# Kernel tuning notes

Hardware: AMD Instinct MI355X
Metric: run time of the kernel (lower is better)

Reference implementation:

```python
import jax, jax.numpy as jnp
import numpy as np

N = 100000      # nodes
E = 1600000     # edges (avg degree 16)
EP = 500000     # pos/neg scored edges
DIN, DH, DOUT = 128, 128, 64


def setup_inputs() -> dict:
    key = jax.random.key(0)
    ks = jax.random.split(key, 8)
    x = jax.random.normal(ks[0], (N, DIN), jnp.float32)
    edge_index = jax.random.randint(ks[1], (2, E), 0, N)
    pos_edge_index = jax.random.randint(ks[2], (2, EP), 0, N)
    neg_edge_index = jax.random.randint(ks[3], (2, EP), 0, N)
    s = lambda k, sh: jax.random.normal(k, sh, jnp.float32) * 0.05
    return dict(
        x=x, edge_index=edge_index,
        pos_edge_index=pos_edge_index, neg_edge_index=neg_edge_index,
        W_l0=s(ks[4], (DIN, DH)), b_l0=jnp.zeros((DH,), jnp.float32), W_r0=s(ks[5], (DIN, DH)),
        W_l1=s(ks[6], (DH, DOUT)), b_l1=jnp.zeros((DOUT,), jnp.float32), W_r1=s(ks[7], (DH, DOUT)),
    )


def sage_conv(h, src, dst, W_l, b_l, W_r):
    # PyG SAGEConv (mean aggr): out_i = W_l @ mean_{j in N(i)} h_j + b_l + W_r @ h_i
    msg = h[src]                                                   # [E, d] gather
    agg = jax.ops.segment_sum(msg, dst, num_segments=h.shape[0])   # [N, d]
    deg = jax.ops.segment_sum(jnp.ones((src.shape[0],), h.dtype), dst, num_segments=h.shape[0])
    mean = agg / jnp.maximum(deg, 1.0)[:, None]
    return mean @ W_l + b_l + h @ W_r


def reference(x, edge_index, pos_edge_index, neg_edge_index,
              W_l0, b_l0, W_r0, W_l1, b_l1, W_r1):
    src, dst = edge_index[0], edge_index[1]
    h = sage_conv(x, src, dst, W_l0, b_l0, W_r0)
    h = jax.nn.relu(h)          # dropout is identity in eval mode
    h = sage_conv(h, src, dst, W_l1, b_l1, W_r1)
    pos_scores = (h[pos_edge_index[0]] * h[pos_edge_index[1]]).sum(axis=1)
    neg_scores = (h[neg_edge_index[0]] * h[neg_edge_index[1]]).sum(axis=1)
    return (pos_scores, neg_scores)
```

## Files before the change

### kernel.cpp

```cpp
#include <hip/hip_runtime.h>

#define NN 100000
#define EE 1600000
#define EPE 500000
#define NBINS 196
#define BCAP 12288
#define EPB 2048
#define NB1 782

typedef short bf8_t __attribute__((ext_vector_type(8)));
typedef float f4_t  __attribute__((ext_vector_type(4)));
typedef float f2v  __attribute__((ext_vector_type(2)));

__device__ __forceinline__ unsigned short f2bf(float f) {
    unsigned u = __float_as_uint(f);
    unsigned r = (u + 0x7fffu + ((u >> 16) & 1u)) >> 16;
    return (unsigned short)r;
}
__device__ __forceinline__ float bfl(unsigned u) { return __uint_as_float(u << 16); }
__device__ __forceinline__ float bfh(unsigned u) { return __uint_as_float(u & 0xffff0000u); }

__device__ __forceinline__ int c0p(int m) {
    return ((m >> 6) & 1) * 64 + (m & 3) * 16 + ((m >> 2) & 15);
}
__device__ __forceinline__ int c1p(int m) {
    return ((m >> 5) & 1) * 32 + (m & 1) * 16 + ((m >> 1) & 15);
}

#if __has_builtin(__builtin_amdgcn_cvt_pk_fp8_f32) && __has_builtin(__builtin_amdgcn_cvt_pk_f32_fp8)
__device__ __forceinline__ unsigned pk4_fp8(float a0, float a1, float a2, float a3) {
    int w = 0;
    w = __builtin_amdgcn_cvt_pk_fp8_f32(a0, a1, w, false);
    w = __builtin_amdgcn_cvt_pk_fp8_f32(a2, a3, w, true);
    return (unsigned)w;
}
__device__ __forceinline__ unsigned short pk2_fp8(float a0, float a1) {
    int w = __builtin_amdgcn_cvt_pk_fp8_f32(a0, a1, 0, false);
    return (unsigned short)(w & 0xffff);
}
__device__ __forceinline__ void accf8(float* a, uint2 v) {
    f2v p0 = __builtin_amdgcn_cvt_pk_f32_fp8((int)v.x, false);
    f2v p1 = __builtin_amdgcn_cvt_pk_f32_fp8((int)v.x, true);
    f2v p2 = __builtin_amdgcn_cvt_pk_f32_fp8((int)v.y, false);
    f2v p3 = __builtin_amdgcn_cvt_pk_f32_fp8((int)v.y, true);
    a[0] += p0.x; a[1] += p0.y; a[2] += p1.x; a[3] += p1.y;
    a[4] += p2.x; a[5] += p2.y; a[6] += p3.x; a[7] += p3.y;
}
#else
#include <hip/hip_fp8.h>
__device__ __forceinline__ unsigned pk4_fp8(float a0, float a1, float a2, float a3) {
    unsigned r;
    r  = (unsigned)__hip_cvt_float_to_fp8(a0, __HIP_SATFINITE, __HIP_E4M3);
    r |= (unsigned)__hip_cvt_float_to_fp8(a1, __HIP_SATFINITE, __HIP_E4M3) << 8;
    r |= (unsigned)__hip_cvt_float_to_fp8(a2, __HIP_SATFINITE, __HIP_E4M3) << 16;
    r |= (unsigned)__hip_cvt_float_to_fp8(a3, __HIP_SATFINITE, __HIP_E4M3) << 24;
    return r;
}
__device__ __forceinline__ unsigned short pk2_fp8(float a0, float a1) {
    unsigned r;
    r  = (unsigned)__hip_cvt_float_to_fp8(a0, __HIP_SATFINITE, __HIP_E4M3);
    r |= (unsigned)__hip_cvt_float_to_fp8(a1, __HIP_SATFINITE, __HIP_E4M3) << 8;
    return (unsigned short)r;
}
__device__ __forceinline__ float dec1_fp8(unsigned b) {
    __hip_fp8_e4m3 h; h.__x = (__hip_fp8_storage_t)(b & 0xff);
    return (float)h;
}
__device__ __forceinline__ void accf8(float* a, uint2 v) {
    a[0] += dec1_fp8(v.x); a[1] += dec1_fp8(v.x >> 8);
    a[2] += dec1_fp8(v.x >> 16); a[3] += dec1_fp8(v.x >> 24);
    a[4] += dec1_fp8(v.y); a[5] += dec1_fp8(v.y >> 8);
    a[6] += dec1_fp8(v.y >> 16); a[7] += dec1_fp8(v.y >> 24);
}
#endif

__global__ __launch_bounds__(256) void binpass1_k(
    const int* __restrict__ src, const int* __restrict__ dst,
    int* __restrict__ bin_cnt, int* __restrict__ binbuf)
{
    __shared__ int cnt_l[NBINS];
    __shared__ int base_l[NBINS];
    int tid = threadIdx.x;
    int e0 = blockIdx.x * EPB;
    for (int i = tid; i < NBINS; i += 256) cnt_l[i] = 0;
    __syncthreads();

    int pk[8];
    #pragma unroll
    for (int i = 0; i < 8; ++i) {
        int e = e0 + tid + i * 256;
        pk[i] = -1;
        if (e < EE) {
            int d = dst[e];
            int b = d >> 9;
            int r = atomicAdd(&cnt_l[b], 1);
            pk[i] = (b << 20) | ((d & 511) << 11) | r;
        }
    }
    __syncthreads();
    for (int i = tid; i < NBINS; i += 256)
        base_l[i] = atomicAdd(&bin_cnt[i], cnt_l[i]);
    __syncthreads();

    #pragma unroll
    for (int i = 0; i < 8; ++i) {
        int e = e0 + tid + i * 256;
        if (e >= EE) continue;
        int v = pk[i];
        int b = v >> 20, dl = (v >> 11) & 511, r = v & 2047;
        binbuf[b * BCAP + base_l[b] + r] = (dl << 17) | src[e];
    }
}

__global__ __launch_bounds__(256) void binpass2_k(
    const int* __restrict__ binbuf, const int* __restrict__ bin_cnt,
    int* __restrict__ csr, int* __restrict__ row_ptr, float* __restrict__ invd)
{
    __shared__ int deg_l[512];
    __shared__ int off_l[512];
    __shared__ int cur_l[512];
    __shared__ int s[256];
    int tid = threadIdx.x;
    int b = blockIdx.x;
    int lo = b << 9;
    int n_here = min(512, NN - lo);

    int bc = (tid < NBINS) ? bin_cnt[tid] : 0;
    s[tid] = bc;
    __syncthreads();
    #pragma unroll
    for (int off = 1; off < 256; off <<= 1) {
        int t = (tid >= off) ? s[tid - off] : 0;
        __syncthreads();
        s[tid] += t;
        __syncthreads();
    }
    int base = (b == 0) ? 0 : s[b - 1];
    int cnt = bin_cnt[b];
    const int* bb = binbuf + b * BCAP;
    __syncthreads();

    deg_l[tid] = 0; deg_l[tid + 256] = 0;
    __syncthreads();
    for (int i = tid; i < cnt; i += 256)
        atomicAdd(&deg_l[bb[i] >> 17], 1);
    __syncthreads();

    int a0 = deg_l[2 * tid], a1 = deg_l[2 * tid + 1];
    s[tid] = a0 + a1;
    __syncthreads();
    #pragma unroll
    for (int off = 1; off < 256; off <<= 1) {
        int t = (tid >= off) ? s[tid - off] : 0;
        __syncthreads();
        s[tid] += t;
        __syncthreads();
    }
    int excl = s[tid] - (a0 + a1);
    off_l[2 * tid] = excl;
    off_l[2 * tid + 1] = excl + a0;
    cur_l[2 * tid] = excl;
    cur_l[2 * tid + 1] = excl + a0;
    __syncthreads();

    for (int j = tid; j < n_here; j += 256) {
        row_ptr[lo + j] = base + off_l[j];
        invd[lo + j] = 1.0f / fmaxf((float)deg_l[j], 1.0f);
    }
    if (tid == 0 && b == NBINS - 1) row_ptr[NN] = EE;

    for (int i = tid; i < cnt; i += 256) {
        int v = bb[i];
        int dstl = v >> 17, srcv = v & 0x1FFFF;
        int pos = atomicAdd(&cur_l[dstl], 1);
        csr[base + pos] = srcv;
    }
}

__global__ void pack_k(const float* __restrict__ Wl0, const float* __restrict__ Wr0,
                       const float* __restrict__ Wl1, const float* __restrict__ Wr1,
                       const float* __restrict__ bl0, const float* __restrict__ bl1,
                       unsigned short* __restrict__ Bp0, unsigned short* __restrict__ Bp1,
                       float* __restrict__ b0p, float* __restrict__ b1p,
                       int* __restrict__ bin_cnt)
{
    int t = blockIdx.x * 256 + threadIdx.x;
    if (t < NBINS) bin_cnt[t] = 0;
    if (t < 4096) {
        int q = t & 3;
        int n = (t >> 2) & 255;
        int kt = t >> 10;
        unsigned short o[8];
        #pragma unroll
        for (int j = 0; j < 8; ++j) {
            int k = kt * 32 + q * 8 + j;
            float v = (n < 128) ? Wl0[(size_t)k * 128 + n] : Wr0[(size_t)k * 128 + (n - 128)];
            o[j] = f2bf(v);
        }
        uint4 w;
        w.x = (unsigned)o[0] | ((unsigned)o[1] << 16);
        w.y = (unsigned)o[2] | ((unsigned)o[3] << 16);
        w.z = (unsigned)o[4] | ((unsigned)o[5] << 16);
        w.w = (unsigned)o[6] | ((unsigned)o[7] << 16);
        *(uint4*)(Bp0 + (size_t)t * 8) = w;
    } else if (t < 6144) {
        int u = t - 4096;
        int q = u & 3;
        int n = (u >> 2) & 127;
        int kt = u >> 9;
        unsigned short o[8];
        #pragma unroll
        for (int j = 0; j < 8; ++j) {
            int k = kt * 32 + q * 8 + j;
            int c = c0p(k);
            float v = (n < 64) ? Wl1[(size_t)c * 64 + n] : Wr1[(size_t)c * 64 + (n - 64)];
            o[j] = f2bf(v);
        }
        uint4 w;
        w.x = (unsigned)o[0] | ((unsigned)o[1] << 16);
        w.y = (unsigned)o[2] | ((unsigned)o[3] << 16);
        w.z = (unsigned)o[4] | ((unsigned)o[5] << 16);
        w.w = (unsigned)o[6] | ((unsigned)o[7] << 16);
        *(uint4*)(Bp1 + (size_t)u * 8) = w;
    } else if (t < 6144 + 128) {
        int m = t - 6144;
        b0p[m] = bl0[c0p(m)];
    } else if (t < 6144 + 192) {
        int m = t - 6272;
        b1p[m] = bl1[c1p(m)];
    }
}

template<int NCOLS, bool AFP32>
__global__ __launch_bounds__(256) void gemm_k(
    const void* __restrict__ Av, const unsigned short* __restrict__ Bp,
    unsigned char* __restrict__ Tout, unsigned short* __restrict__ Rout)
{
    constexpr int STRIP = NCOLS / 4;
    constexpr int NT = STRIP / 16;
    constexpr int HC = NCOLS / 2;
    int w = threadIdx.x >> 6;
    int lane = threadIdx.x & 63;
    int ln = lane & 15, q = lane >> 4;
    int half = w >> 1, wsub = w & 1;
    int row0 = blockIdx.x * 64;
    int colbase = half * HC + wsub * STRIP;

    bf8_t Bf[4][NT];
    #pragma unroll
    for (int kt = 0; kt < 4; ++kt)
        #pragma unroll
        for (int nt = 0; nt < NT; ++nt)
            Bf[kt][nt] = *(const bf8_t*)(Bp + (size_t)kt * NCOLS * 32
                                         + (size_t)(colbase + nt * 16 + ln) * 32 + q * 8);

    for (int rt = 0; rt < 4; ++rt) {
        int rowt = row0 + rt * 16;
        if (rowt >= NN) break;
        int arow = rowt + ln;

        bf8_t Af[4];
        if (AFP32) {
            #pragma unroll
            for (int kt = 0; kt < 4; ++kt) {
                const float* ap = (const float*)Av + (size_t)arow * 128 + kt * 32 + q * 8;
                f4_t a0 = *(const f4_t*)ap;
                f4_t a1 = *(const f4_t*)(ap + 4);
                #pragma unroll
                for (int j = 0; j < 4; ++j) {
                    Af[kt][j]     = (short)f2bf(a0[j]);
                    Af[kt][4 + j] = (short)f2bf(a1[j]);
                }
            }
        } else {
            #pragma unroll
            for (int kt = 0; kt < 4; ++kt)
                Af[kt] = *(const bf8_t*)((const unsigned short*)Av
                                         + (size_t)arow * 128 + kt * 32 + q * 8);
        }

        f4_t acc[NT];
        #pragma unroll
        for (int nt = 0; nt < NT; ++nt) acc[nt] = (f4_t){0.f, 0.f, 0.f, 0.f};
        #pragma unroll
        for (int kt = 0; kt < 4; ++kt)
            #pragma unroll
            for (int nt = 0; nt < NT; ++nt)
                acc[nt] = __builtin_amdgcn_mfma_f32_16x16x32_bf16(Af[kt], Bf[kt][nt], acc[nt], 0, 0, 0);

        #pragma unroll
        for (int r = 0; r < 4; ++r) {
            int row = rowt + q * 4 + r;
            if (half == 0) {
                if (NT == 4) {
                    unsigned v = pk4_fp8(acc[0][r], acc[1][r], acc[2][r], acc[3][r]);
                    *(unsigned*)(Tout + (size_t)row * HC + wsub * 64 + ln * 4) = v;
                } else {
                    unsigned short v = pk2_fp8(acc[0][r], acc[1][r]);
                    *(unsigned short*)(Tout + (size_t)row * HC + wsub * 32 + ln * 2) = v;
                }
            } else {
                if (NT == 4) {
                    uint2 v;
                    v.x = (unsigned)f2bf(acc[0][r]) | ((unsigned)f2bf(acc[1][r]) << 16);
                    v.y = (unsigned)f2bf(acc[2][r]) | ((unsigned)f2bf(acc[3][r]) << 16);
                    *(uint2*)(Rout + (size_t)row * HC + wsub * 64 + ln * 4) = v;
                } else {
                    unsigned v = (unsigned)f2bf(acc[0][r]) | ((unsigned)f2bf(acc[1][r]) << 16);
                    *(unsigned*)(Rout + (size_t)row * HC + wsub * 32 + ln * 2) = v;
                }
            }
        }
    }
}

__device__ __forceinline__ void unp8(float* a, uint4 v) {
    a[0] = bfl(v.x); a[1] = bfh(v.x);
    a[2] = bfl(v.y); a[3] = bfh(v.y);
    a[4] = bfl(v.z); a[5] = bfh(v.z);
    a[6] = bfl(v.w); a[7] = bfh(v.w);
}

template<int LPNS, bool RELU>
__global__ __launch_bounds__(256) void gather_fuse_k(
    const unsigned char* __restrict__ tq, const int* __restrict__ csr,
    const int* __restrict__ row_ptr, const float* __restrict__ invd,
    const unsigned short* __restrict__ rg, const float* __restrict__ biasp,
    unsigned short* __restrict__ hout)
{
    constexpr int STRIDE = 8 << LPNS;
    int t = blockIdx.x * 256 + threadIdx.x;
    int node = t >> LPNS;
    int lane = t & ((1 << LPNS) - 1);
    if (node >= NN) return;
    int e = row_ptr[node];
    int e1 = row_ptr[node + 1];
    const unsigned char* fb = tq + lane * 8;

    float a0[8] = {0.f, 0.f, 0.f, 0.f, 0.f, 0.f, 0.f, 0.f};
    float a1[8] = {0.f, 0.f, 0.f, 0.f, 0.f, 0.f, 0.f, 0.f};
    for (; e + 3 < e1; e += 4) {
        int s0 = csr[e], s1 = csr[e + 1], s2 = csr[e + 2], s3 = csr[e + 3];
        uint2 v0 = *(const uint2*)(fb + (size_t)s0 * STRIDE);
        uint2 v1 = *(const uint2*)(fb + (size_t)s1 * STRIDE);
        uint2 v2 = *(const uint2*)(fb + (size_t)s2 * STRIDE);
        uint2 v3 = *(const uint2*)(fb + (size_t)s3 * STRIDE);
        accf8(a0, v0); accf8(a1, v1); accf8(a0, v2); accf8(a1, v3);
    }
    for (; e < e1; ++e) {
        int s0 = csr[e];
        uint2 v0 = *(const uint2*)(fb + (size_t)s0 * STRIDE);
        accf8(a0, v0);
    }

    float inv = invd[node];
    uint4 rv = *(const uint4*)(rg + (size_t)node * STRIDE + lane * 8);
    float rr[8];
    unp8(rr, rv);
    f4_t b0 = *(const f4_t*)(biasp + lane * 8);
    f4_t b1 = *(const f4_t*)(biasp + lane * 8 + 4);
    float o[8];
    #pragma unroll
    for (int j = 0; j < 8; ++j) {
        float bj = (j < 4) ? b0[j] : b1[j - 4];
        float v = (a0[j] + a1[j]) * inv + rr[j] + bj;
        o[j] = RELU ? fmaxf(v, 0.f) : v;
    }
    uint4 w;
    w.x = (unsigned)f2bf(o[0]) | ((unsigned)f2bf(o[1]) << 16);
    w.y = (unsigned)f2bf(o[2]) | ((unsigned)f2bf(o[3]) << 16);
    w.z = (unsigned)f2bf(o[4]) | ((unsigned)f2bf(o[5]) << 16);
    w.w = (unsigned)f2bf(o[6]) | ((unsigned)f2bf(o[7]) << 16);
    *(uint4*)(hout + (size_t)node * STRIDE + lane * 8) = w;
}

__device__ __forceinline__ float dot8(uint4 va, uint4 vb) {
    return bfl(va.x) * bfl(vb.x) + bfh(va.x) * bfh(vb.x)
         + bfl(va.y) * bfl(vb.y) + bfh(va.y) * bfh(vb.y)
         + bfl(va.z) * bfl(vb.z) + bfh(va.z) * bfh(vb.z)
         + bfl(va.w) * bfl(vb.w) + bfh(va.w) * bfh(vb.w);
}

__global__ __launch_bounds__(256) void score_k(
    const unsigned short* __restrict__ h2b, const int* __restrict__ pos,
    const int* __restrict__ neg, float* __restrict__ out)
{
    int t = blockIdx.x * 256 + threadIdx.x;
    int g = t >> 3, l = t & 7;
    int eg0 = g * 2;
    if (eg0 >= 2 * EPE) return;
    int eg1 = eg0 + 1;
    int a0i, b0i, a1i, b1i;
    if (eg0 < EPE) { a0i = pos[eg0]; b0i = pos[EPE + eg0]; }
    else { int e2 = eg0 - EPE; a0i = neg[e2]; b0i = neg[EPE + e2]; }
    if (eg1 < EPE) { a1i = pos[eg1]; b1i = pos[EPE + eg1]; }
    else { int e2 = eg1 - EPE; a1i = neg[e2]; b1i = neg[EPE + e2]; }
    const unsigned short* hb = h2b + (size_t)l * 8;
    uint4 va0 = *(const uint4*)(hb + (size_t)a0i * 64);
    uint4 vb0 = *(const uint4*)(hb + (size_t)b0i * 64);
    uint4 va1 = *(const uint4*)(hb + (size_t)a1i * 64);
    uint4 vb1 = *(const uint4*)(hb + (size_t)b1i * 64);
    float p0 = dot8(va0, vb0);
    float p1 = dot8(va1, vb1);
    p0 += __shfl_xor(p0, 1, 8);
    p1 += __shfl_xor(p1, 1, 8);
    p0 += __shfl_xor(p0, 2, 8);
    p1 += __shfl_xor(p1, 2, 8);
    p0 += __shfl_xor(p0, 4, 8);
    p1 += __shfl_xor(p1, 4, 8);
    if (l == 0) { out[eg0] = p0; out[eg1] = p1; }
}

extern "C" void kernel_launch(void* const* d_in, const int* in_sizes, int n_in,
                              void* d_out, int out_size, void* d_ws, size_t ws_size,
                              hipStream_t stream) {
    const float* x   = (const float*)d_in[0];
    const int*   ei  = (const int*)d_in[1];
    const int*   pei = (const int*)d_in[2];
    const int*   nei = (const int*)d_in[3];
    const float* Wl0 = (const float*)d_in[4];
    const float* bl0 = (const float*)d_in[5];
    const float* Wr0 = (const float*)d_in[6];
    const float* Wl1 = (const float*)d_in[7];
    const float* bl1 = (const float*)d_in[8];
    const float* Wr1 = (const float*)d_in[9];
    float* out = (float*)d_out;

    char* ws = (char*)d_ws;
    size_t off = 0;
    auto alloc = [&](size_t bytes) {
        void* p = ws + off;
        off = (off + bytes + 255) & ~(size_t)255;
        return p;
    };
    float* invd     = (float*)alloc((size_t)NN * 4);
    int*   row_ptr  = (int*)  alloc((size_t)(NN + 1) * 4);
    int*   bin_cnt  = (int*)  alloc((size_t)NBINS * 4);
    int*   binbuf   = (int*)  alloc((size_t)NBINS * BCAP * 4);
    int*   csr      = (int*)  alloc((size_t)EE * 4);
    unsigned short* Bp0 = (unsigned short*)alloc((size_t)4096 * 8 * 2);
    unsigned short* Bp1 = (unsigned short*)alloc((size_t)2048 * 8 * 2);
    float* b0p = (float*)alloc(128 * 4);
    float* b1p = (float*)alloc(64 * 4);
    unsigned char*  t0q = (unsigned char*) alloc((size_t)NN * 128);
    unsigned short* r0b = (unsigned short*)alloc((size_t)NN * 128 * 2);
    unsigned short* h1b = (unsigned short*)alloc((size_t)NN * 128 * 2);
    unsigned char*  t1q = t0q;
    unsigned short* r1b = r0b;
    unsigned short* h2b = h1b;

    const int* src = ei;
    const int* dst = ei + EE;

    pack_k<<<25, 256, 0, stream>>>(Wl0, Wr0, Wl1, Wr1, bl0, bl1, Bp0, Bp1, b0p, b1p, bin_cnt);
    binpass1_k<<<NB1, 256, 0, stream>>>(src, dst, bin_cnt, binbuf);
    binpass2_k<<<NBINS, 256, 0, stream>>>(binbuf, bin_cnt, csr, row_ptr, invd);

    gemm_k<256, true><<<1563, 256, 0, stream>>>(x, Bp0, t0q, r0b);
    gather_fuse_k<4, true><<<(NN * 16 + 255) / 256, 256, 0, stream>>>(
        t0q, csr, row_ptr, invd, r0b, b0p, h1b);

    gemm_k<128, false><<<1563, 256, 0, stream>>>(h1b, Bp1, t1q, r1b);
    gather_fuse_k<3, false><<<(NN * 8 + 255) / 256, 256, 0, stream>>>(
        t1q, csr, row_ptr, invd, r1b, b1p, h2b);

    score_k<<<(EPE * 8 + 255) / 256, 256, 0, stream>>>(h2b, pei, nei, out);
}
```

Baseline: 297.9 us.

## Merge prep kernels horizontally and overlap CSR build with first GEMM

Several small launches are combined into horizontally fused kernels. Edge binning, weight packing and a new fp32-to-bf16 conversion of x now share one launch, and the second binning pass runs alongside the first GEMM in another. The GEMM tile grows from 64 to 128 rows per block with a fully unrolled row loop, and the bin counter reset moves to a memset. The aim is to cut launch gaps and tail idle time by overlapping independent stages. The cost is an extra bf16 copy of x written to and read back from memory, plus higher register pressure in the GEMM.

```diff
diff --git a/kernel.cpp b/kernel.cpp
--- a/kernel.cpp
+++ b/kernel.cpp
@@ -7,6 +7,8 @@
 #define BCAP 12288
 #define EPB 2048
 #define NB1 782
+#define GEMMB 782
+#define CONVB 6250
 
 typedef short bf8_t __attribute__((ext_vector_type(8)));
 typedef float f4_t  __attribute__((ext_vector_type(4)));
@@ -74,14 +76,14 @@
 }
 #endif
 
-__global__ __launch_bounds__(256) void binpass1_k(
-    const int* __restrict__ src, const int* __restrict__ dst,
-    int* __restrict__ bin_cnt, int* __restrict__ binbuf)
+__device__ void binpass1_body(int blk, const int* __restrict__ src,
+                              const int* __restrict__ dst,
+                              int* __restrict__ bin_cnt, int* __restrict__ binbuf)
 {
     __shared__ int cnt_l[NBINS];
     __shared__ int base_l[NBINS];
     int tid = threadIdx.x;
-    int e0 = blockIdx.x * EPB;
+    int e0 = blk * EPB;
     for (int i = tid; i < NBINS; i += 256) cnt_l[i] = 0;
     __syncthreads();
 
@@ -112,16 +114,15 @@
     }
 }
 
-__global__ __launch_bounds__(256) void binpass2_k(
-    const int* __restrict__ binbuf, const int* __restrict__ bin_cnt,
-    int* __restrict__ csr, int* __restrict__ row_ptr, float* __restrict__ invd)
+__device__ void binpass2_body(int b, const int* __restrict__ binbuf,
+                              const int* __restrict__ bin_cnt, int* __restrict__ csr,
+                              int* __restrict__ row_ptr, float* __restrict__ invd)
 {
     __shared__ int deg_l[512];
     __shared__ int off_l[512];
     __shared__ int cur_l[512];
     __shared__ int s[256];
     int tid = threadIdx.x;
-    int b = blockIdx.x;
     int lo = b << 9;
     int n_here = min(512, NN - lo);
 
@@ -177,15 +178,13 @@
     }
 }
 
-__global__ void pack_k(const float* __restrict__ Wl0, const float* __restrict__ Wr0,
-                       const float* __restrict__ Wl1, const float* __restrict__ Wr1,
-                       const float* __restrict__ bl0, const float* __restrict__ bl1,
-                       unsigned short* __restrict__ Bp0, unsigned short* __restrict__ Bp1,
-                       float* __restrict__ b0p, float* __restrict__ b1p,
-                       int* __restrict__ bin_cnt)
-{
-    int t = blockIdx.x * 256 + threadIdx.x;
-    if (t < NBINS) bin_cnt[t] = 0;
+__device__ void pack_body(int blk, const float* __restrict__ Wl0, const float* __restrict__ Wr0,
+                          const float* __restrict__ Wl1, const float* __restrict__ Wr1,
+                          const float* __restrict__ bl0, const float* __restrict__ bl1,
+                          unsigned short* __restrict__ Bp0, unsigned short* __restrict__ Bp1,
+                          float* __restrict__ b0p, float* __restrict__ b1p)
+{
+    int t = blk * 256 + threadIdx.x;
     if (t < 4096) {
         int q = t & 3;
         int n = (t >> 2) & 255;
@@ -231,9 +230,22 @@
     }
 }
 
-template<int NCOLS, bool AFP32>
-__global__ __launch_bounds__(256) void gemm_k(
-    const void* __restrict__ Av, const unsigned short* __restrict__ Bp,
+__device__ void conv_body(int blk, const float* __restrict__ x, unsigned short* __restrict__ xb)
+{
+    int i = blk * 256 + threadIdx.x;
+    const float4* xp = (const float4*)x + (size_t)i * 2;
+    float4 a = xp[0], b = xp[1];
+    uint4 w;
+    w.x = (unsigned)f2bf(a.x) | ((unsigned)f2bf(a.y) << 16);
+    w.y = (unsigned)f2bf(a.z) | ((unsigned)f2bf(a.w) << 16);
+    w.z = (unsigned)f2bf(b.x) | ((unsigned)f2bf(b.y) << 16);
+    w.w = (unsigned)f2bf(b.z) | ((unsigned)f2bf(b.w) << 16);
+    *(uint4*)(xb + (size_t)i * 8) = w;
+}
+
+template<int NCOLS>
+__device__ __forceinline__ void gemm_body(
+    int blk, const unsigned short* __restrict__ Ab, const unsigned short* __restrict__ Bp,
     unsigned char* __restrict__ Tout, unsigned short* __restrict__ Rout)
 {
     constexpr int STRIP = NCOLS / 4;
@@ -243,7 +255,7 @@
     int lane = threadIdx.x & 63;
     int ln = lane & 15, q = lane >> 4;
     int half = w >> 1, wsub = w & 1;
-    int row0 = blockIdx.x * 64;
+    int row0 = blk * 128;
     int colbase = half * HC + wsub * STRIP;
 
     bf8_t Bf[4][NT];
@@ -254,64 +266,87 @@
             Bf[kt][nt] = *(const bf8_t*)(Bp + (size_t)kt * NCOLS * 32
                                          + (size_t)(colbase + nt * 16 + ln) * 32 + q * 8);
 
-    for (int rt = 0; rt < 4; ++rt) {
+    #pragma unroll
+    for (int rt = 0; rt < 8; ++rt) {
         int rowt = row0 + rt * 16;
-        if (rowt >= NN) break;
-        int arow = rowt + ln;
-
-        bf8_t Af[4];
-        if (AFP32) {
-            #pragma unroll
-            for (int kt = 0; kt < 4; ++kt) {
-                const float* ap = (const float*)Av + (size_t)arow * 128 + kt * 32 + q * 8;
-                f4_t a0 = *(const f4_t*)ap;
-                f4_t a1 = *(const f4_t*)(ap + 4);
-                #pragma unroll
-                for (int j = 0; j < 4; ++j) {
-                    Af[kt][j]     = (short)f2bf(a0[j]);
-                    Af[kt][4 + j] = (short)f2bf(a1[j]);
-                }
-            }
-        } else {
+        if (rowt < NN) {
+            int arow = rowt + ln;
+            bf8_t Af[4];
             #pragma unroll
             for (int kt = 0; kt < 4; ++kt)
-                Af[kt] = *(const bf8_t*)((const unsigned short*)Av
-                                         + (size_t)arow * 128 + kt * 32 + q * 8);
-        }
-
-        f4_t acc[NT];
-        #pragma unroll
-        for (int nt = 0; nt < NT; ++nt) acc[nt] = (f4_t){0.f, 0.f, 0.f, 0.f};
-        #pragma unroll
-        for (int kt = 0; kt < 4; ++kt)
+                Af[kt] = *(const bf8_t*)(Ab + (size_t)arow * 128 + kt * 32 + q * 8);
+
+            f4_t acc[NT];
             #pragma unroll
-            for (int nt = 0; nt < NT; ++nt)
-                acc[nt] = __builtin_amdgcn_mfma_f32_16x16x32_bf16(Af[kt], Bf[kt][nt], acc[nt], 0, 0, 0);
-
-        #pragma unroll
-        for (int r = 0; r < 4; ++r) {
-            int row = rowt + q * 4 + r;
-            if (half == 0) {
-                if (NT == 4) {
-                    unsigned v = pk4_fp8(acc[0][r], acc[1][r], acc[2][r], acc[3][r]);
-                    *(unsigned*)(Tout + (size_t)row * HC + wsub * 64 + ln * 4) = v;
+            for (int nt = 0; nt < NT; ++nt) acc[nt] = (f4_t){0.f, 0.f, 0.f, 0.f};
+            #pragma unroll
+            for (int kt = 0; kt < 4; ++kt)
+                #pragma unroll
+                for (int nt = 0; nt < NT; ++nt)
+                    acc[nt] = __builtin_amdgcn_mfma_f32_16x16x32_bf16(Af[kt], Bf[kt][nt], acc[nt], 0, 0, 0);
+
+            #pragma unroll
+            for (int r = 0; r < 4; ++r) {
+                int row = rowt + q * 4 + r;
+                if (half == 0) {
+                    if (NT == 4) {
+                        unsigned v = pk4_fp8(acc[0][r], acc[1][r], acc[2][r], acc[3][r]);
+                        *(unsigned*)(Tout + (size_t)row * HC + wsub * 64 + ln * 4) = v;
+                    } else {
+                        unsigned short v = pk2_fp8(acc[0][r], acc[1][r]);
+                        *(unsigned short*)(Tout + (size_t)row * HC + wsub * 32 + ln * 2) = v;
+                    }
                 } else {
-                    unsigned short v = pk2_fp8(acc[0][r], acc[1][r]);
-                    *(unsigned short*)(Tout + (size_t)row * HC + wsub * 32 + ln * 2) = v;
-                }
-            } else {
-                if (NT == 4) {
-                    uint2 v;
-                    v.x = (unsigned)f2bf(acc[0][r]) | ((unsigned)f2bf(acc[1][r]) << 16);
-                    v.y = (unsigned)f2bf(acc[2][r]) | ((unsigned)f2bf(acc[3][r]) << 16);
-                    *(uint2*)(Rout + (size_t)row * HC + wsub * 64 + ln * 4) = v;
-                } else {
-                    unsigned v = (unsigned)f2bf(acc[0][r]) | ((unsigned)f2bf(acc[1][r]) << 16);
-                    *(unsigned*)(Rout + (size_t)row * HC + wsub * 32 + ln * 2) = v;
+                    if (NT == 4) {
+                        uint2 v;
+                        v.x = (unsigned)f2bf(acc[0][r]) | ((unsigned)f2bf(acc[1][r]) << 16);
+                        v.y = (unsigned)f2bf(acc[2][r]) | ((unsigned)f2bf(acc[3][r]) << 16);
+                        *(uint2*)(Rout + (size_t)row * HC + wsub * 64 + ln * 4) = v;
+                    } else {
+                        unsigned v = (unsigned)f2bf(acc[0][r]) | ((unsigned)f2bf(acc[1][r]) << 16);
+                        *(unsigned*)(Rout + (size_t)row * HC + wsub * 32 + ln * 2) = v;
+                    }
                 }
             }
         }
     }
+}
+
+__global__ __launch_bounds__(256) void prep_k(
+    const int* __restrict__ src, const int* __restrict__ dst,
+    int* __restrict__ bin_cnt, int* __restrict__ binbuf,
+    const float* __restrict__ x, unsigned short* __restrict__ xb,
+    const float* __restrict__ Wl0, const float* __restrict__ Wr0,
+    const float* __restrict__ Wl1, const float* __restrict__ Wr1,
+    const float* __restrict__ bl0, const float* __restrict__ bl1,
+    unsigned short* __restrict__ Bp0, unsigned short* __restrict__ Bp1,
+    float* __restrict__ b0p, float* __restrict__ b1p)
+{
+    if (blockIdx.x < NB1)
+        binpass1_body(blockIdx.x, src, dst, bin_cnt, binbuf);
+    else if (blockIdx.x < NB1 + 25)
+        pack_body(blockIdx.x - NB1, Wl0, Wr0, Wl1, Wr1, bl0, bl1, Bp0, Bp1, b0p, b1p);
+    else
+        conv_body(blockIdx.x - NB1 - 25, x, xb);
+}
+
+__global__ __launch_bounds__(256) void gemm0_bp2_k(
+    const unsigned short* __restrict__ xb, const unsigned short* __restrict__ Bp0,
+    unsigned char* __restrict__ t0q, unsigned short* __restrict__ r0b,
+    const int* __restrict__ binbuf, const int* __restrict__ bin_cnt,
+    int* __restrict__ csr, int* __restrict__ row_ptr, float* __restrict__ invd)
+{
+    if (blockIdx.x < GEMMB)
+        gemm_body<256>(blockIdx.x, xb, Bp0, t0q, r0b);
+    else
+        binpass2_body(blockIdx.x - GEMMB, binbuf, bin_cnt, csr, row_ptr, invd);
+}
+
+__global__ __launch_bounds__(256) void gemm1_k(
+    const unsigned short* __restrict__ h1b, const unsigned short* __restrict__ Bp1,
+    unsigned char* __restrict__ t1q, unsigned short* __restrict__ r1b)
+{
+    gemm_body<128>(blockIdx.x, h1b, Bp1, t1q, r1b);
 }
 
 __device__ __forceinline__ void unp8(float* a, uint4 v) {
@@ -442,6 +477,7 @@
     unsigned short* Bp1 = (unsigned short*)alloc((size_t)2048 * 8 * 2);
     float* b0p = (float*)alloc(128 * 4);
     float* b1p = (float*)alloc(64 * 4);
+    unsigned short* xb  = (unsigned short*)alloc((size_t)NN * 128 * 2);
     unsigned char*  t0q = (unsigned char*) alloc((size_t)NN * 128);
     unsigned short* r0b = (unsigned short*)alloc((size_t)NN * 128 * 2);
     unsigned short* h1b = (unsigned short*)alloc((size_t)NN * 128 * 2);
@@ -452,15 +488,20 @@
     const int* src = ei;
     const int* dst = ei + EE;
 
-    pack_k<<<25, 256, 0, stream>>>(Wl0, Wr0, Wl1, Wr1, bl0, bl1, Bp0, Bp1, b0p, b1p, bin_cnt);
-    binpass1_k<<<NB1, 256, 0, stream>>>(src, dst, bin_cnt, binbuf);
-    binpass2_k<<<NBINS, 256, 0, stream>>>(binbuf, bin_cnt, csr, row_ptr, invd);
-
-    gemm_k<256, true><<<1563, 256, 0, stream>>>(x, Bp0, t0q, r0b);
+    hipMemsetAsync(bin_cnt, 0, (size_t)NBINS * 4, stream);
+
+    prep_k<<<NB1 + 25 + CONVB, 256, 0, stream>>>(
+        src, dst, bin_cnt, binbuf, x, xb,
+        Wl0, Wr0, Wl1, Wr1, bl0, bl1, Bp0, Bp1, b0p, b1p);
+
+    gemm0_bp2_k<<<GEMMB + NBINS, 256, 0, stream>>>(
+        xb, Bp0, t0q, r0b, binbuf, bin_cnt, csr, row_ptr, invd);
+
     gather_fuse_k<4, true><<<(NN * 16 + 255) / 256, 256, 0, stream>>>(
         t0q, csr, row_ptr, invd, r0b, b0p, h1b);
 
-    gemm_k<128, false><<<1563, 256, 0, stream>>>(h1b, Bp1, t1q, r1b);
+    gemm1_k<<<GEMMB, 256, 0, stream>>>(h1b, Bp1, t1q, r1b);
+
     gather_fuse_k<3, false><<<(NN * 8 + 255) / 256, 256, 0, stream>>>(
         t1q, csr, row_ptr, invd, r1b, b1p, h2b);
 
```

Result: faster. 284.3 us (-4.6%).
